# Optimization experiments

Measured on AMD Instinct MI355X. Metric: run time of the kernel, lower is better.

## Reference

```python
import jax, jax.numpy as jnp
import numpy as np

WIN_LEN = 3072
HOP = 192


def hann_window(n):
    # torch.hann_window(n, periodic=False)
    k = jnp.arange(n, dtype=jnp.float32)
    return 0.5 - 0.5 * jnp.cos(2.0 * jnp.pi * k / (n - 1))


def setup_inputs() -> dict:
    key = jax.random.key(0)
    k1, k2 = jax.random.split(key)
    B, C, F, T = 8, 1, 128, 1000
    filter_bands = jax.random.uniform(k1, (B, C, F, T), dtype=jnp.float32)
    # torch: rand*2-1 uniform in [-1, 1)
    noise = jax.random.uniform(k2, (B, C, (T - 1) * HOP), dtype=jnp.float32) * 2.0 - 1.0
    return {"filter_bands": filter_bands, "noise": noise}


def reference(filter_bands, noise):
    B, C, F, T = filter_bands.shape
    half = WIN_LEN // 2  # 1536
    padded = jnp.pad(noise, ((0, 0), (0, 0), (half, half)))
    L = padded.shape[-1]  # (T-1)*HOP + 2*half
    # unfold: [T, WIN_LEN] gather indices, frames [B, C, T, WIN_LEN]
    frame_idx = jnp.arange(T)[:, None] * HOP + jnp.arange(WIN_LEN)[None, :]
    frames = padded[:, :, frame_idx]
    # nearest interpolation of bands F -> half (torch 'nearest': floor(i*F/out))
    src = (jnp.arange(half) * F) // half
    filt = filter_bands[:, :, src, :]          # [B, C, half, T]
    filt = jnp.transpose(filt, (0, 1, 3, 2))   # [B, C, T, half]
    filt = jnp.pad(filt, ((0, 0), (0, 0), (0, 0), (1, 0)))  # prepend DC zero -> half+1 bins
    spec = jnp.fft.rfft(frames)                # [B, C, T, half+1] complex
    out_frames = jnp.fft.irfft(filt * spec, n=WIN_LEN)  # [B, C, T, WIN_LEN]
    out_frames = out_frames * hann_window(WIN_LEN)
    # overlap-add (F.fold with stride HOP)
    out = jnp.zeros((B, C, L), dtype=out_frames.dtype)
    out = out.at[:, :, frame_idx.reshape(-1)].add(out_frames.reshape(B, C, -1))
    return out[:, :, half:-half]
```

## Files before the change

### kernel.cpp

```cpp
#include <hip/hip_runtime.h>

#define NFFT 3072
#define THREADS 256
#define HOP 192
#define HALF 1536
#define TFRAMES 1000
#define OUTLEN 191808
#define NBANDS 128
#define PI_F 3.14159265358979323846f

__device__ __forceinline__ float2 cadd(float2 a,float2 b){return make_float2(a.x+b.x,a.y+b.y);}
__device__ __forceinline__ float2 csub(float2 a,float2 b){return make_float2(a.x-b.x,a.y-b.y);}
__device__ __forceinline__ float2 cmul(float2 a,float2 b){
    return make_float2(fmaf(a.x,b.x,-a.y*b.y), fmaf(a.x,b.y,a.y*b.x));
}
__device__ __forceinline__ float2 cmuln_i(float2 a){return make_float2(a.y,-a.x);}
__device__ __forceinline__ float2 cneg(float2 a){return make_float2(-a.x,-a.y);}

__device__ __forceinline__ int IDX(int i){ return i + (i>>4); }

__device__ __forceinline__ void dft4(float2 a0,float2 a1,float2 a2,float2 a3,
                                     float2&y0,float2&y1,float2&y2,float2&y3){
    float2 e0=cadd(a0,a2), e1=csub(a0,a2), o0=cadd(a1,a3), o1=csub(a1,a3);
    y0=cadd(e0,o0); y2=csub(e0,o0);
    float2 io=make_float2(-o1.y,o1.x);
    y1=csub(e1,io); y3=cadd(e1,io);
}
__device__ __forceinline__ void dft3(float2 a0,float2 a1,float2 a2,
                                     float2&y0,float2&y1,float2&y2){
    float2 s=cadd(a1,a2), d=csub(a1,a2);
    y0=cadd(a0,s);
    float2 t=make_float2(a0.x-0.5f*s.x, a0.y-0.5f*s.y);
    const float S3=0.86602540378443864676f;
    float2 id=make_float2(S3*d.y,-S3*d.x);
    y1=cadd(t,id); y2=csub(t,id);
}

__device__ __forceinline__ void dft12(float2 a[12], float2 o[12]){
    float2 u[3][4];
    #pragma unroll
    for(int n2=0;n2<3;++n2)
        dft4(a[n2],a[3+n2],a[6+n2],a[9+n2],u[n2][0],u[n2][1],u[n2][2],u[n2][3]);
    const float2 W1=make_float2( 0.86602540378443865f,-0.5f);
    const float2 W2=make_float2( 0.5f,-0.86602540378443865f);
    const float2 W4=make_float2(-0.5f,-0.86602540378443865f);
    u[1][1]=cmul(u[1][1],W1); u[1][2]=cmul(u[1][2],W2); u[1][3]=cmuln_i(u[1][3]);
    u[2][1]=cmul(u[2][1],W2); u[2][2]=cmul(u[2][2],W4); u[2][3]=cneg(u[2][3]);
    #pragma unroll
    for(int k1=0;k1<4;++k1)
        dft3(u[0][k1],u[1][k1],u[2][k1], o[k1],o[k1+4],o[k1+8]);
}

__device__ __forceinline__ void dft16(float2 a[16], float2 o[16]){
    float2 u[4][4];
    #pragma unroll
    for(int n2=0;n2<4;++n2)
        dft4(a[n2],a[4+n2],a[8+n2],a[12+n2],u[n2][0],u[n2][1],u[n2][2],u[n2][3]);
    const float C16=0.92387953251128674f, S16=0.38268343236508977f, R2=0.70710678118654752f;
    const float2 W1=make_float2( C16,-S16), W2=make_float2( R2,-R2), W3=make_float2( S16,-C16);
    const float2 W6=make_float2(-R2,-R2),  W9=make_float2(-C16, S16);
    u[1][1]=cmul(u[1][1],W1); u[1][2]=cmul(u[1][2],W2);   u[1][3]=cmul(u[1][3],W3);
    u[2][1]=cmul(u[2][1],W2); u[2][2]=cmuln_i(u[2][2]);   u[2][3]=cmul(u[2][3],W6);
    u[3][1]=cmul(u[3][1],W3); u[3][2]=cmul(u[3][2],W6);   u[3][3]=cmul(u[3][3],W9);
    #pragma unroll
    for(int k1=0;k1<4;++k1)
        dft4(u[0][k1],u[1][k1],u[2][k1],u[3][k1], o[k1],o[k1+4],o[k1+8],o[k1+12]);
}

template<int R>
__device__ __forceinline__ void twiddle_pows(float2* o, float ang){
    float s,c; __sincosf(ang,&s,&c);
    float2 w1=make_float2(c,s);
    float2 w2=cmul(w1,w1);
    float2 w3=cmul(w2,w1);
    float2 w4=cmul(w2,w2);
    o[1]=cmul(o[1],w1); o[2]=cmul(o[2],w2); o[3]=cmul(o[3],w3);
    float2 w8=cmul(w4,w4);
    float2 w5=cmul(w4,w1), w6=cmul(w4,w2), w7=cmul(w4,w3);
    o[4]=cmul(o[4],w4); o[5]=cmul(o[5],w5); o[6]=cmul(o[6],w6); o[7]=cmul(o[7],w7);
    float2 w9=cmul(w8,w1), w10=cmul(w8,w2), w11=cmul(w8,w3);
    o[8]=cmul(o[8],w8); o[9]=cmul(o[9],w9); o[10]=cmul(o[10],w10); o[11]=cmul(o[11],w11);
    if constexpr (R>12){
        float2 w12=cmul(w8,w4), w13=cmul(w8,w5), w14=cmul(w8,w6), w15=cmul(w8,w7);
        o[12]=cmul(o[12],w12); o[13]=cmul(o[13],w13); o[14]=cmul(o[14],w14); o[15]=cmul(o[15],w15);
    }
}

__device__ __forceinline__ void stageB(float2* A, int tid){
    const bool act = tid < 192;
    float2 o[16];
    int q=0,p=0;
    if(act){
        q = tid % 12; p = tid / 12;
        float2 a[16];
        int ib = IDX(q + 12*p);
        #pragma unroll
        for(int l=0;l<16;++l) a[l] = A[ib + 204*l];
        dft16(a,o);
        twiddle_pows<16>(o, -2.0f*PI_F*(float)p*(1.0f/256.0f));
    }
    __syncthreads();
    if(act){
        #pragma unroll
        for(int j=0;j<16;++j) A[IDX(q + 192*p + 12*j)] = o[j];
    }
    __syncthreads();
}

__global__ __launch_bounds__(THREADS,4)
void filtered_noise_kernel(const float* __restrict__ fb,
                           const float* __restrict__ noise,
                           float* __restrict__ out)
{
    __shared__ float2 A[NFFT + NFFT/16];
    __shared__ float gf[2*NBANDS];

    const int tid = threadIdx.x;
    const int wg  = blockIdx.x;
    const int b   = wg / (TFRAMES/2);
    const int tp  = wg % (TFRAMES/2);
    const int t0  = 2*tp;
    const float* nz = noise + (size_t)b * OUTLEN;
    const int base0 = t0*HOP - HALF;

    gf[tid] = fb[((size_t)b*NBANDS + (tid & 127))*TFRAMES + t0 + (tid >> 7)];

    {
        float2 a[12], o[12];
        #pragma unroll
        for(int l=0;l<12;++l){
            int i0 = base0 + tid + 256*l;
            float x0 = (i0 >= 0 && i0 < OUTLEN) ? nz[i0] : 0.0f;
            int i1 = i0 + HOP;
            float x1 = (i1 >= 0 && i1 < OUTLEN) ? nz[i1] : 0.0f;
            a[l] = make_float2(x0, x1);
        }
        dft12(a,o);
        twiddle_pows<12>(o, -2.0f*PI_F*(float)tid*(1.0f/3072.0f));
        #pragma unroll
        for(int j=0;j<12;++j) A[IDX(12*tid + j)] = o[j];
    }
    __syncthreads();

    stageB(A, tid);

    {
        const bool act = tid < 192;
        float2 o[16];
        if(act){
            float2 a[16];
            int ib = IDX(tid);
            #pragma unroll
            for(int l=0;l<16;++l) a[l] = A[ib + 204*l];
            dft16(a,o);
        }
        __syncthreads();
        if(act){
            int ib = IDX(tid);
            #pragma unroll
            for(int j=0;j<16;++j) A[ib + 204*j] = o[j];
        }
        __syncthreads();
    }

    {
        const int p = tid;
        float2 z[12], zm[12];
        {
            int ib = IDX(p);
            #pragma unroll
            for(int l=0;l<12;++l) z[l] = A[ib + 272*l];
        }
        {
            int pm = (p==0) ? 0 : (256 - p);
            int ib = IDX(pm);
            #pragma unroll
            for(int l=0;l<12;++l) zm[l] = A[ib + 272*l];
        }
        float2 w[12];
        #pragma unroll
        for(int l=0;l<12;++l){
            int k = p + 256*l;
            int j = (k <= HALF) ? k : (NFFT - k);
            float aa = 0.0f, bb = 0.0f;
            if(j){
                int band = (j-1)/12;
                float Gx = gf[band], Gy = gf[NBANDS + band];
                aa = 0.5f*(Gx+Gy); bb = 0.5f*(Gx-Gy);
            }
            float2 Zm = (p==0) ? ((l==0) ? z[0] : z[12-l]) : zm[11-l];
            w[l] = make_float2( fmaf(aa, z[l].x,  bb*Zm.x),
                                fmaf(-aa, z[l].y, bb*Zm.y) );
        }
        float2 o[12];
        dft12(w,o);
        twiddle_pows<12>(o, -2.0f*PI_F*(float)p*(1.0f/3072.0f));
        __syncthreads();
        #pragma unroll
        for(int j=0;j<12;++j) A[IDX(12*p + j)] = o[j];
        __syncthreads();
    }

    stageB(A, tid);

    {
        const bool act = tid < 192;
        if(act){
            float2 a[16], o[16];
            int ib = IDX(tid);
            #pragma unroll
            for(int l=0;l<16;++l) a[l] = A[ib + 204*l];
            dft16(a,o);
            const float invN = 1.0f/(float)NFFT;
            float* outb = out + (size_t)b * OUTLEN;
            #pragma unroll
            for(int j=0;j<16;++j){
                int n = tid + 192*j;
                float h = 0.5f - 0.5f*__cosf(2.0f*PI_F*(float)n*(1.0f/3071.0f));
                float s = invN*h;
                float vx =  o[j].x * s;
                float vy = -o[j].y * s;
                int p0 = base0 + n;
                if(p0 >= 0 && p0 < OUTLEN) atomicAdd(&outb[p0], vx);
                int p1 = p0 + HOP;
                if(p1 >= 0 && p1 < OUTLEN) atomicAdd(&outb[p1], vy);
            }
        }
    }
}

extern "C" void kernel_launch(void* const* d_in, const int* in_sizes, int n_in,
                              void* d_out, int out_size, void* d_ws, size_t ws_size,
                              hipStream_t stream)
{
    const float* fb    = (const float*)d_in[0];
    const float* noise = (const float*)d_in[1];
    float* out = (float*)d_out;

    int B = in_sizes[1] / OUTLEN;

    hipMemsetAsync(out, 0, (size_t)out_size * sizeof(float), stream);

    dim3 grid(B * (TFRAMES/2));
    filtered_noise_kernel<<<grid, THREADS, 0, stream>>>(fb, noise, out);
}
```

Baseline: 159.4 us.

## Pre-combine frame pair overlap in shared memory before global atomics

```diff
diff --git a/kernel.cpp b/kernel.cpp
--- a/kernel.cpp
+++ b/kernel.cpp
@@ -8,6 +8,7 @@
 #define OUTLEN 191808
 #define NBANDS 128
 #define PI_F 3.14159265358979323846f
+#define OLA_LEN 3456
 
 __device__ __forceinline__ float2 cadd(float2 a,float2 b){return make_float2(a.x+b.x,a.y+b.y);}
 __device__ __forceinline__ float2 csub(float2 a,float2 b){return make_float2(a.x-b.x,a.y-b.y);}
@@ -116,9 +117,8 @@
     __shared__ float gf[2*NBANDS];
 
     const int tid = threadIdx.x;
-    const int wg  = blockIdx.x;
-    const int b   = wg / (TFRAMES/2);
-    const int tp  = wg % (TFRAMES/2);
+    const int b   = blockIdx.x & 7;
+    const int tp  = blockIdx.x >> 3;
     const int t0  = 2*tp;
     const float* nz = noise + (size_t)b * OUTLEN;
     const int base0 = t0*HOP - HALF;
@@ -205,25 +205,45 @@
 
     {
         const bool act = tid < 192;
-        if(act){
-            float2 a[16], o[16];
+        float2 o[16];
+        float vy[16];
+        if(act){
+            float2 a[16];
             int ib = IDX(tid);
             #pragma unroll
             for(int l=0;l<16;++l) a[l] = A[ib + 204*l];
             dft16(a,o);
+        }
+        __syncthreads();
+        float* C = (float*)A;
+        if (tid < 128){ C[3072+tid]=0.0f; C[3200+tid]=0.0f; C[3328+tid]=0.0f; }
+        if(act){
             const float invN = 1.0f/(float)NFFT;
-            float* outb = out + (size_t)b * OUTLEN;
             #pragma unroll
             for(int j=0;j<16;++j){
                 int n = tid + 192*j;
                 float h = 0.5f - 0.5f*__cosf(2.0f*PI_F*(float)n*(1.0f/3071.0f));
                 float s = invN*h;
-                float vx =  o[j].x * s;
-                float vy = -o[j].y * s;
-                int p0 = base0 + n;
-                if(p0 >= 0 && p0 < OUTLEN) atomicAdd(&outb[p0], vx);
-                int p1 = p0 + HOP;
-                if(p1 >= 0 && p1 < OUTLEN) atomicAdd(&outb[p1], vy);
+                C[n]  =  o[j].x * s;
+                vy[j] = -o[j].y * s;
+            }
+        }
+        __syncthreads();
+        if(act){
+            #pragma unroll
+            for(int j=0;j<16;++j){
+                int n = tid + 192*j;
+                C[n + HOP] += vy[j];
+            }
+        }
+        __syncthreads();
+        float* outb = out + (size_t)b * OUTLEN;
+        #pragma unroll
+        for(int j=0;j<14;++j){
+            int c = tid + 256*j;
+            if (c < OLA_LEN){
+                int p0 = base0 + c;
+                if (p0 >= 0 && p0 < OUTLEN) atomicAdd(&outb[p0], C[c]);
             }
         }
     }
```

Result: faster. 155.1 us (-2.7%).

## Replace atomic overlap-add with per-segment workspace writes and a gather reduction kernel

Applied to the files above, without the earlier changes.

```diff
diff --git a/kernel.cpp b/kernel.cpp
--- a/kernel.cpp
+++ b/kernel.cpp
@@ -8,6 +8,8 @@
 #define OUTLEN 191808
 #define NBANDS 128
 #define PI_F 3.14159265358979323846f
+#define SEGLEN 3264
+#define NSEG 500
 
 __device__ __forceinline__ float2 cadd(float2 a,float2 b){return make_float2(a.x+b.x,a.y+b.y);}
 __device__ __forceinline__ float2 csub(float2 a,float2 b){return make_float2(a.x-b.x,a.y-b.y);}
@@ -107,18 +109,19 @@
     __syncthreads();
 }
 
+template<bool USE_WS>
 __global__ __launch_bounds__(THREADS,4)
 void filtered_noise_kernel(const float* __restrict__ fb,
                            const float* __restrict__ noise,
+                           float* __restrict__ ws,
                            float* __restrict__ out)
 {
     __shared__ float2 A[NFFT + NFFT/16];
     __shared__ float gf[2*NBANDS];
 
     const int tid = threadIdx.x;
-    const int wg  = blockIdx.x;
-    const int b   = wg / (TFRAMES/2);
-    const int tp  = wg % (TFRAMES/2);
+    const int b   = blockIdx.x & 7;
+    const int tp  = blockIdx.x >> 3;
     const int t0  = 2*tp;
     const float* nz = noise + (size_t)b * OUTLEN;
     const int base0 = t0*HOP - HALF;
@@ -212,21 +215,47 @@
             for(int l=0;l<16;++l) a[l] = A[ib + 204*l];
             dft16(a,o);
             const float invN = 1.0f/(float)NFFT;
-            float* outb = out + (size_t)b * OUTLEN;
-            #pragma unroll
-            for(int j=0;j<16;++j){
-                int n = tid + 192*j;
-                float h = 0.5f - 0.5f*__cosf(2.0f*PI_F*(float)n*(1.0f/3071.0f));
-                float s = invN*h;
-                float vx =  o[j].x * s;
-                float vy = -o[j].y * s;
-                int p0 = base0 + n;
-                if(p0 >= 0 && p0 < OUTLEN) atomicAdd(&outb[p0], vx);
-                int p1 = p0 + HOP;
-                if(p1 >= 0 && p1 < OUTLEN) atomicAdd(&outb[p1], vy);
+            float prev_vy = 0.0f;
+            float* seg = USE_WS ? (ws + (size_t)(b*NSEG + tp)*SEGLEN) : nullptr;
+            float* outb = USE_WS ? nullptr : (out + (size_t)b*OUTLEN);
+            #pragma unroll
+            for(int j=0;j<17;++j){
+                int c = tid + 192*j;
+                float val = prev_vy;
+                if (j < 16){
+                    float h = 0.5f - 0.5f*__cosf(2.0f*PI_F*(float)c*(1.0f/3071.0f));
+                    float s = invN*h;
+                    val    += o[j].x * s;
+                    prev_vy = -o[j].y * s;
+                }
+                if (USE_WS){
+                    seg[c] = val;
+                } else {
+                    int p0 = base0 + c;
+                    if (p0 >= 0 && p0 < OUTLEN) atomicAdd(&outb[p0], val);
+                }
             }
         }
     }
+}
+
+__global__ __launch_bounds__(256)
+void ola_reduce_kernel(const float* __restrict__ ws, float* __restrict__ out)
+{
+    const int n = blockIdx.x*256 + threadIdx.x;
+    const int b = blockIdx.y;
+    if (n >= OUTLEN) return;
+    int tp1 = (n + 1536) / 384;            if (tp1 > NSEG-1) tp1 = NSEG-1;
+    int tp0 = (n > 1727) ? (n - 1344) / 384 : 0;
+    const float* wb = ws + (size_t)b*NSEG*SEGLEN;
+    float s = 0.0f;
+    #pragma unroll
+    for (int i = 0; i < 9; ++i){
+        int tp = tp0 + i;
+        if (tp <= tp1)
+            s += wb[tp*SEGLEN + (n + 1536 - 384*tp)];
+    }
+    out[(size_t)b*OUTLEN + n] = s;
 }
 
 extern "C" void kernel_launch(void* const* d_in, const int* in_sizes, int n_in,
@@ -237,10 +266,19 @@
     const float* noise = (const float*)d_in[1];
     float* out = (float*)d_out;
 
-    int B = in_sizes[1] / OUTLEN;
-
-    hipMemsetAsync(out, 0, (size_t)out_size * sizeof(float), stream);
-
-    dim3 grid(B * (TFRAMES/2));
-    filtered_noise_kernel<<<grid, THREADS, 0, stream>>>(fb, noise, out);
-}
+    const int B = in_sizes[1] / OUTLEN;
+    const size_t need = (size_t)B * NSEG * SEGLEN * sizeof(float);
+
+    dim3 grid1(B * NSEG);
+
+    if (ws_size >= need){
+        filtered_noise_kernel<true><<<grid1, THREADS, 0, stream>>>(
+            fb, noise, (float*)d_ws, out);
+        dim3 grid2((OUTLEN + 255)/256, B);
+        ola_reduce_kernel<<<grid2, 256, 0, stream>>>((float*)d_ws, out);
+    } else {
+        hipMemsetAsync(out, 0, (size_t)out_size * sizeof(float), stream);
+        filtered_noise_kernel<false><<<grid1, THREADS, 0, stream>>>(
+            fb, noise, nullptr, out);
+    }
+}
```

Result: faster. 155.2 us (-2.6%).

## Process four frame pairs per block with register overlap-add accumulation

Applied to the files above, without the earlier changes.

```diff
diff --git a/kernel.cpp b/kernel.cpp
--- a/kernel.cpp
+++ b/kernel.cpp
@@ -8,6 +8,8 @@
 #define OUTLEN 191808
 #define NBANDS 128
 #define PI_F 3.14159265358979323846f
+#define NPAIR 4
+#define NSB 125
 
 __device__ __forceinline__ float2 cadd(float2 a,float2 b){return make_float2(a.x+b.x,a.y+b.y);}
 __device__ __forceinline__ float2 csub(float2 a,float2 b){return make_float2(a.x-b.x,a.y-b.y);}
@@ -113,118 +115,151 @@
                            float* __restrict__ out)
 {
     __shared__ float2 A[NFFT + NFFT/16];
-    __shared__ float gf[2*NBANDS];
+    __shared__ float gfs[NBANDS*2*NPAIR];
 
     const int tid = threadIdx.x;
-    const int wg  = blockIdx.x;
-    const int b   = wg / (TFRAMES/2);
-    const int tp  = wg % (TFRAMES/2);
-    const int t0  = 2*tp;
+    const int b   = blockIdx.x & 7;
+    const int sb  = blockIdx.x >> 3;
+    const int T0  = sb * (2*NPAIR);
     const float* nz = noise + (size_t)b * OUTLEN;
-    const int base0 = t0*HOP - HALF;
-
-    gf[tid] = fb[((size_t)b*NBANDS + (tid & 127))*TFRAMES + t0 + (tid >> 7)];
-
+    const int blockbase = T0*HOP - HALF;
+
+    #pragma unroll
+    for(int i=0;i<4;++i){
+        int idx = tid + 256*i;
+        int f = idx >> 3, ft = idx & 7;
+        gfs[idx] = fb[((size_t)b*NBANDS + f)*TFRAMES + T0 + ft];
+    }
+
+    const bool act = tid < 192;
+    float hw[16];
     {
-        float2 a[12], o[12];
-        #pragma unroll
-        for(int l=0;l<12;++l){
-            int i0 = base0 + tid + 256*l;
-            float x0 = (i0 >= 0 && i0 < OUTLEN) ? nz[i0] : 0.0f;
-            int i1 = i0 + HOP;
-            float x1 = (i1 >= 0 && i1 < OUTLEN) ? nz[i1] : 0.0f;
-            a[l] = make_float2(x0, x1);
-        }
-        dft12(a,o);
-        twiddle_pows<12>(o, -2.0f*PI_F*(float)tid*(1.0f/3072.0f));
-        #pragma unroll
-        for(int j=0;j<12;++j) A[IDX(12*tid + j)] = o[j];
-    }
-    __syncthreads();
-
-    stageB(A, tid);
-
-    {
-        const bool act = tid < 192;
-        float2 o[16];
-        if(act){
-            float2 a[16];
-            int ib = IDX(tid);
-            #pragma unroll
-            for(int l=0;l<16;++l) a[l] = A[ib + 204*l];
-            dft16(a,o);
-        }
+        const float invN = 1.0f/(float)NFFT;
+        #pragma unroll
+        for(int j=0;j<16;++j){
+            int n = tid + 192*j;
+            hw[j] = invN*(0.5f - 0.5f*__cosf(2.0f*PI_F*(float)n*(1.0f/3071.0f)));
+        }
+    }
+
+    float acc[17];
+    #pragma unroll
+    for(int d=0;d<17;++d) acc[d]=0.0f;
+
+    float* outb = out + (size_t)b * OUTLEN;
+
+    for(int pi=0; pi<NPAIR; ++pi){
+        const int t0 = T0 + 2*pi;
+        const int base0 = t0*HOP - HALF;
+        const int tt = 2*pi;
+
         __syncthreads();
-        if(act){
-            int ib = IDX(tid);
-            #pragma unroll
-            for(int j=0;j<16;++j) A[ib + 204*j] = o[j];
+
+        {
+            float2 a[12], o[12];
+            #pragma unroll
+            for(int l=0;l<12;++l){
+                int i0 = base0 + tid + 256*l;
+                float x0 = (i0 >= 0 && i0 < OUTLEN) ? nz[i0] : 0.0f;
+                int i1 = i0 + HOP;
+                float x1 = (i1 >= 0 && i1 < OUTLEN) ? nz[i1] : 0.0f;
+                a[l] = make_float2(x0, x1);
+            }
+            dft12(a,o);
+            twiddle_pows<12>(o, -2.0f*PI_F*(float)tid*(1.0f/3072.0f));
+            #pragma unroll
+            for(int j=0;j<12;++j) A[IDX(12*tid + j)] = o[j];
         }
         __syncthreads();
-    }
-
-    {
-        const int p = tid;
-        float2 z[12], zm[12];
+
+        stageB(A, tid);
+
         {
-            int ib = IDX(p);
-            #pragma unroll
-            for(int l=0;l<12;++l) z[l] = A[ib + 272*l];
-        }
+            float2 o[16];
+            if(act){
+                float2 a[16];
+                int ib = IDX(tid);
+                #pragma unroll
+                for(int l=0;l<16;++l) a[l] = A[ib + 204*l];
+                dft16(a,o);
+            }
+            __syncthreads();
+            if(act){
+                int ib = IDX(tid);
+                #pragma unroll
+                for(int j=0;j<16;++j) A[ib + 204*j] = o[j];
+            }
+            __syncthreads();
+        }
+
         {
-            int pm = (p==0) ? 0 : (256 - p);
-            int ib = IDX(pm);
-            #pragma unroll
-            for(int l=0;l<12;++l) zm[l] = A[ib + 272*l];
-        }
-        float2 w[12];
-        #pragma unroll
-        for(int l=0;l<12;++l){
-            int k = p + 256*l;
-            int j = (k <= HALF) ? k : (NFFT - k);
-            float aa = 0.0f, bb = 0.0f;
-            if(j){
-                int band = (j-1)/12;
-                float Gx = gf[band], Gy = gf[NBANDS + band];
-                aa = 0.5f*(Gx+Gy); bb = 0.5f*(Gx-Gy);
-            }
-            float2 Zm = (p==0) ? ((l==0) ? z[0] : z[12-l]) : zm[11-l];
-            w[l] = make_float2( fmaf(aa, z[l].x,  bb*Zm.x),
-                                fmaf(-aa, z[l].y, bb*Zm.y) );
-        }
-        float2 o[12];
-        dft12(w,o);
-        twiddle_pows<12>(o, -2.0f*PI_F*(float)p*(1.0f/3072.0f));
-        __syncthreads();
-        #pragma unroll
-        for(int j=0;j<12;++j) A[IDX(12*p + j)] = o[j];
-        __syncthreads();
-    }
-
-    stageB(A, tid);
-
-    {
-        const bool act = tid < 192;
+            const int p = tid;
+            float2 z[12], zm[12];
+            {
+                int ib = IDX(p);
+                #pragma unroll
+                for(int l=0;l<12;++l) z[l] = A[ib + 272*l];
+            }
+            {
+                int pm = (p==0) ? 0 : (256 - p);
+                int ib = IDX(pm);
+                #pragma unroll
+                for(int l=0;l<12;++l) zm[l] = A[ib + 272*l];
+            }
+            float2 w[12];
+            #pragma unroll
+            for(int l=0;l<12;++l){
+                int k = p + 256*l;
+                int j = (k <= HALF) ? k : (NFFT - k);
+                float aa = 0.0f, bb = 0.0f;
+                if(j){
+                    int band = (j-1)/12;
+                    float Gx = gfs[(band<<3) + tt];
+                    float Gy = gfs[(band<<3) + tt + 1];
+                    aa = 0.5f*(Gx+Gy); bb = 0.5f*(Gx-Gy);
+                }
+                float2 Zm = (p==0) ? ((l==0) ? z[0] : z[12-l]) : zm[11-l];
+                w[l] = make_float2( fmaf(aa, z[l].x,  bb*Zm.x),
+                                    fmaf(-aa, z[l].y, bb*Zm.y) );
+            }
+            float2 o[12];
+            dft12(w,o);
+            twiddle_pows<12>(o, -2.0f*PI_F*(float)p*(1.0f/3072.0f));
+            __syncthreads();
+            #pragma unroll
+            for(int j=0;j<12;++j) A[IDX(12*p + j)] = o[j];
+            __syncthreads();
+        }
+
+        stageB(A, tid);
+
         if(act){
             float2 a[16], o[16];
             int ib = IDX(tid);
             #pragma unroll
             for(int l=0;l<16;++l) a[l] = A[ib + 204*l];
             dft16(a,o);
-            const float invN = 1.0f/(float)NFFT;
-            float* outb = out + (size_t)b * OUTLEN;
             #pragma unroll
             for(int j=0;j<16;++j){
-                int n = tid + 192*j;
-                float h = 0.5f - 0.5f*__cosf(2.0f*PI_F*(float)n*(1.0f/3071.0f));
-                float s = invN*h;
-                float vx =  o[j].x * s;
-                float vy = -o[j].y * s;
-                int p0 = base0 + n;
-                if(p0 >= 0 && p0 < OUTLEN) atomicAdd(&outb[p0], vx);
-                int p1 = p0 + HOP;
-                if(p1 >= 0 && p1 < OUTLEN) atomicAdd(&outb[p1], vy);
-            }
+                float s = hw[j];
+                acc[j]   = fmaf( o[j].x, s, acc[j]);
+                acc[j+1] = fmaf(-o[j].y, s, acc[j+1]);
+            }
+            int p0 = blockbase + tid + 192*tt;
+            if (p0 >= 0 && p0 < OUTLEN) atomicAdd(&outb[p0], acc[0]);
+            int p1 = p0 + HOP;
+            if (p1 >= 0 && p1 < OUTLEN) atomicAdd(&outb[p1], acc[1]);
+        }
+        #pragma unroll
+        for(int d=0;d<15;++d) acc[d] = acc[d+2];
+        acc[15]=0.0f; acc[16]=0.0f;
+    }
+
+    if(act){
+        #pragma unroll
+        for(int d=0;d<15;++d){
+            int p = blockbase + tid + 192*(2*NPAIR + d);
+            if (p >= 0 && p < OUTLEN) atomicAdd(&outb[p], acc[d]);
         }
     }
 }
@@ -237,10 +272,10 @@
     const float* noise = (const float*)d_in[1];
     float* out = (float*)d_out;
 
-    int B = in_sizes[1] / OUTLEN;
+    const int B = in_sizes[1] / OUTLEN;
 
     hipMemsetAsync(out, 0, (size_t)out_size * sizeof(float), stream);
 
-    dim3 grid(B * (TFRAMES/2));
+    dim3 grid(B * NSB);
     filtered_noise_kernel<<<grid, THREADS, 0, stream>>>(fb, noise, out);
 }
```

New measurement: 264.5 us. 65.9% more time.
